# Kernel tuning notes

Hardware: AMD Instinct MI355X
Metric: run time of the kernel (lower is better)

Reference implementation:

```python
import jax, jax.numpy as jnp
import numpy as np

LN_EPS = 1e-5
RMS_EPS = 1e-5

B, T, D = 4, 2048, 1024
H, DK, DV = 4, 256, 512            # head_k_dim = D/H, head_v_dim = expand_v * head_k_dim (expand_v=2)
KDIM, VDIM = H * DK, H * DV        # 1024, 2048
FFN = 4096                          # int(d_model * ffn_ratio)
CONV = 4


def _layernorm(x, w, b):
    mu = jnp.mean(x, -1, keepdims=True)
    var = jnp.mean(jnp.square(x - mu), -1, keepdims=True)
    return (x - mu) * jax.lax.rsqrt(var + LN_EPS) * w + b


def _short_conv_silu(x, w):
    # causal depthwise conv, kernel size K, then SiLU. x: [B,T,C], w: [C,K]
    K = w.shape[1]
    xp = jnp.pad(x, ((0, 0), (K - 1, 0), (0, 0)))
    y = sum(xp[:, i:i + x.shape[1], :] * w[:, i] for i in range(K))
    return jax.nn.silu(y)


def _l2norm(x):
    return x * jax.lax.rsqrt(jnp.sum(jnp.square(x), -1, keepdims=True) + 1e-6)


def _gated_delta_rule(q, k, v, g, beta):
    # q,k: [B,T,H,DK]; v: [B,T,H,DV]; g,beta: [B,T,H]
    # S_t = exp(g_t)*S_{t-1} + k_t (beta_t*(v_t - k_t^T exp(g_t) S_{t-1}))^T ; o_t = q_t^T S_t
    def step(S, inp):
        qt, kt, vt, gt, bt = inp
        S = S * jnp.exp(gt)[..., None, None]          # [B,H,DK,DV]
        mem = jnp.einsum('bhk,bhkv->bhv', kt, S)
        delta = (vt - mem) * bt[..., None]
        S = S + jnp.einsum('bhk,bhv->bhkv', kt, delta)
        o = jnp.einsum('bhk,bhkv->bhv', qt, S)
        return S, o
    S0 = jnp.zeros((q.shape[0], H, DK, DV), q.dtype)
    xs = (q.transpose(1, 0, 2, 3), k.transpose(1, 0, 2, 3), v.transpose(1, 0, 2, 3),
          g.transpose(1, 0, 2), beta.transpose(1, 0, 2))
    _, o = jax.lax.scan(step, S0, xs)
    return o.transpose(1, 0, 2, 3)  # [B,T,H,DV]


def setup_inputs() -> dict:
    key = jax.random.key(0)
    ks = jax.random.split(key, 24)
    n = lambda k, shp, s=0.02: jax.random.normal(k, shp, dtype=jnp.float32) * s
    return {
        'x': jax.random.normal(ks[0], (B, T, D), dtype=jnp.float32),
        'Wq': n(ks[1], (D, KDIM)), 'Wk': n(ks[2], (D, KDIM)), 'Wv': n(ks[3], (D, VDIM)),
        'Wa': n(ks[4], (D, H)), 'Wb': n(ks[5], (D, H)), 'Wg': n(ks[6], (D, VDIM)),
        'conv_q_w': n(ks[7], (KDIM, CONV), 0.2), 'conv_k_w': n(ks[8], (KDIM, CONV), 0.2),
        'conv_v_w': n(ks[9], (VDIM, CONV), 0.2),
        'A_log': jnp.log(jax.random.uniform(ks[10], (H,), minval=1.0, maxval=16.0, dtype=jnp.float32)),
        'dt_bias': jax.random.uniform(ks[11], (H,), minval=0.0, maxval=0.5, dtype=jnp.float32),
        'o_norm_w': jnp.ones((DV,), jnp.float32),
        'Wo': n(ks[12], (VDIM, D)),
        'ln1_w': jnp.ones((D,), jnp.float32), 'ln1_b': jnp.zeros((D,), jnp.float32),
        'ln2_w': jnp.ones((D,), jnp.float32), 'ln2_b': jnp.zeros((D,), jnp.float32),
        'ffn_w1': n(ks[13], (D, FFN)), 'ffn_b1': jnp.zeros((FFN,), jnp.float32),
        'ffn_w2': n(ks[14], (FFN, D)), 'ffn_b2': jnp.zeros((D,), jnp.float32),
    }


def reference(x, Wq, Wk, Wv, Wa, Wb, Wg, conv_q_w, conv_k_w, conv_v_w, A_log, dt_bias,
              o_norm_w, Wo, ln1_w, ln1_b, ln2_w, ln2_b, ffn_w1, ffn_b1, ffn_w2, ffn_b2):
    normed = _layernorm(x, ln1_w, ln1_b)
    q = _short_conv_silu(normed @ Wq, conv_q_w).reshape(B, T, H, DK)
    k = _short_conv_silu(normed @ Wk, conv_k_w).reshape(B, T, H, DK)
    v = _short_conv_silu(normed @ Wv, conv_v_w).reshape(B, T, H, DV)
    q = _l2norm(q) * (DK ** -0.5)
    k = _l2norm(k)
    g = -jnp.exp(A_log) * jax.nn.softplus(normed @ Wa + dt_bias)   # [B,T,H], negative
    beta = jax.nn.sigmoid(normed @ Wb)                              # [B,T,H]
    o = _gated_delta_rule(q, k, v, g, beta)                         # [B,T,H,DV]
    gate = (normed @ Wg).reshape(B, T, H, DV)
    o = o * jax.lax.rsqrt(jnp.mean(jnp.square(o), -1, keepdims=True) + RMS_EPS)
    o = o * o_norm_w * jax.nn.silu(gate)                            # gated RMSNorm
    x = x + o.reshape(B, T, VDIM) @ Wo
    h = _layernorm(x, ln2_w, ln2_b)
    ffn = jax.nn.gelu(h @ ffn_w1 + ffn_b1, approximate=False) @ ffn_w2 + ffn_b2
    return x + ffn
```

## Files before the change

### kernel.cpp

```cpp
#include <hip/hip_runtime.h>
#include <math.h>

#define B_    4
#define T_    2048
#define D_    1024
#define H_    4
#define DK_   256
#define DV_   512
#define KDIM_ 1024
#define VDIM_ 2048
#define FFN_  4096
#define BT_   8192

typedef unsigned short bf16;
typedef __attribute__((ext_vector_type(8))) short short8;
typedef __attribute__((ext_vector_type(4))) short short4v;
typedef __attribute__((ext_vector_type(4))) float f32x4;


__device__ __forceinline__ float sigmoidf_(float x) { return 1.f / (1.f + expf(-x)); }
__device__ __forceinline__ float siluf_(float x)    { return x / (1.f + expf(-x)); }
__device__ __forceinline__ float geluf_(float x)    { return 0.5f * x * (1.f + erff(x * 0.70710678118654752f)); }

__device__ __forceinline__ float bf2f(bf16 u) {
  union { unsigned int i; float f; } c; c.i = (unsigned int)u << 16; return c.f;
}
__device__ __forceinline__ bf16 f2bf(float f) {
  union { unsigned int i; float f; } c; c.f = f;
  unsigned int r = c.i + 0x7fffu + ((c.i >> 16) & 1u);
  return (bf16)(r >> 16);
}

__device__ __forceinline__ void gload16(const bf16* g, bf16* l) {
  __builtin_amdgcn_global_load_lds((__attribute__((address_space(1))) const void*)g,
                                   (__attribute__((address_space(3))) void*)l, 16, 0, 0);
}

__device__ __forceinline__ void storeC(float* p, float v) { *p = v; }
__device__ __forceinline__ void storeC(bf16* p, float v)  { *p = f2bf(v); }

__device__ __forceinline__ short8 ld76(const bf16* p) {
  union { short8 v; short4v h[2]; } u;
  u.h[0] = *(const short4v*)p;
  u.h[1] = *(const short4v*)(p + 4);
  return u.v;
}
__device__ __forceinline__ void st4bf(bf16* p, f32x4 v) {
  short4v o;
  o[0] = (short)f2bf(v[0]); o[1] = (short)f2bf(v[1]);
  o[2] = (short)f2bf(v[2]); o[3] = (short)f2bf(v[3]);
  *(short4v*)p = o;
}

__device__ __forceinline__ float block_sum256(float v, float* red) {
#pragma unroll
  for (int off = 32; off; off >>= 1) v += __shfl_xor(v, off, 64);
  __syncthreads();
  if ((threadIdx.x & 63) == 0) red[threadIdx.x >> 6] = v;
  __syncthreads();
  return red[0] + red[1] + red[2] + red[3];
}


__global__ __launch_bounds__(256) void sentinel_kernel(float* out, int n) {
  int i = blockIdx.x * 256 + threadIdx.x;
  if (i < n) out[i] = 12345.0f;
}


__global__ __launch_bounds__(256) void ln_kernel(const float* __restrict__ x,
                                                 const float* __restrict__ w,
                                                 const float* __restrict__ b,
                                                 bf16* __restrict__ y) {
  __shared__ float red[4];
  int row = blockIdx.x;
  const float* xr = x + (size_t)row * D_;
  float xv[4];
  float s = 0.f;
#pragma unroll
  for (int i = 0; i < 4; i++) { xv[i] = xr[threadIdx.x + 256 * i]; s += xv[i]; }
  float mean = block_sum256(s, red) * (1.f / D_);
  float s2 = 0.f;
#pragma unroll
  for (int i = 0; i < 4; i++) { float d = xv[i] - mean; s2 += d * d; }
  float var = block_sum256(s2, red) * (1.f / D_);
  float inv = rsqrtf(var + 1e-5f);
  bf16* yr = y + (size_t)row * D_;
#pragma unroll
  for (int i = 0; i < 4; i++) {
    int c = threadIdx.x + 256 * i;
    yr[c] = f2bf((xv[i] - mean) * inv * w[c] + b[c]);
  }
}


__global__ __launch_bounds__(256) void convT_kernel(const float* __restrict__ src,
                                                    bf16* __restrict__ dst,
                                                    int K, int N) {
  __shared__ float t[32][33];
  int n0 = blockIdx.x * 32, k0 = blockIdx.y * 32;
  int tx = threadIdx.x & 31, ty = threadIdx.x >> 5;
#pragma unroll
  for (int i = 0; i < 4; i++)
    t[ty + i * 8][tx] = src[(size_t)(k0 + ty + i * 8) * N + n0 + tx];
  __syncthreads();
#pragma unroll
  for (int i = 0; i < 4; i++)
    dst[(size_t)(n0 + ty + i * 8) * K + k0 + tx] = f2bf(t[tx][ty + i * 8]);
}


__global__ __launch_bounds__(256) void kT_kernel(const bf16* __restrict__ k16,
                                                 bf16* __restrict__ kT) {
  __shared__ bf16 tile[32][34];
  int t0 = blockIdx.x * 32;
  int d0 = blockIdx.y * 32;
  int bh = blockIdx.z;
  int b = bh >> 2, h = bh & 3;
  int tx = threadIdx.x & 31, ty = threadIdx.x >> 5;
#pragma unroll
  for (int i = 0; i < 4; i++)
    tile[ty + 8 * i][tx] = k16[(size_t)(b * T_ + t0 + ty + 8 * i) * KDIM_ + h * DK_ + d0 + tx];
  __syncthreads();
#pragma unroll
  for (int i = 0; i < 4; i++)
    kT[((size_t)bh * DK_ + d0 + ty + 8 * i) * T_ + t0 + tx] = tile[tx][ty + 8 * i];
}


template <typename TC>
__global__ __launch_bounds__(256) void gemm_mfma(const bf16* __restrict__ A,
                                                 const bf16* __restrict__ Bt,
                                                 const float* __restrict__ bias,
                                                 const float* __restrict__ res,
                                                 TC* __restrict__ C,
                                                 int N, int K, int flags) {
  __shared__ __align__(16) bf16 As[128 * 32];
  __shared__ __align__(16) bf16 Bs[128 * 32];
  int tid = threadIdx.x;
  int wave = tid >> 6, lane = tid & 63;
  int bm = blockIdx.y * 128, bn = blockIdx.x * 128;
  int wm = (wave >> 1) * 64, wn = (wave & 1) * 64;
  int lm = lane & 15;
  int quad = lane >> 4;

  f32x4 acc[4][4];
#pragma unroll
  for (int i = 0; i < 4; i++)
#pragma unroll
    for (int j = 0; j < 4; j++) acc[i][j] = (f32x4){0.f, 0.f, 0.f, 0.f};

  int srow = wave * 32 + (lane >> 2);
  int scol = (lane & 3) * 8;
  const bf16* ag = A  + (size_t)(bm + srow) * K + scol;
  const bf16* bg = Bt + (size_t)(bn + srow) * K + scol;
  bf16* al = As + wave * 32 * 32;
  bf16* bl = Bs + wave * 32 * 32;
  const size_t gstep = (size_t)16 * K;

  for (int k0 = 0; k0 < K; k0 += 32) {
    gload16(ag + k0,         al);
    gload16(ag + k0 + gstep, al + 16 * 32);
    gload16(bg + k0,         bl);
    gload16(bg + k0 + gstep, bl + 16 * 32);
    __syncthreads();

    short8 af[4], bf[4];
#pragma unroll
    for (int i = 0; i < 4; i++)
      af[i] = *(const short8*)&As[(wm + i * 16 + lm) * 32 + quad * 8];
#pragma unroll
    for (int j = 0; j < 4; j++)
      bf[j] = *(const short8*)&Bs[(wn + j * 16 + lm) * 32 + quad * 8];
#pragma unroll
    for (int i = 0; i < 4; i++)
#pragma unroll
      for (int j = 0; j < 4; j++)
        acc[i][j] = __builtin_amdgcn_mfma_f32_16x16x32_bf16(af[i], bf[j], acc[i][j], 0, 0, 0);
    __syncthreads();
  }

#pragma unroll
  for (int i = 0; i < 4; i++) {
    int row0 = bm + wm + i * 16 + quad * 4;
#pragma unroll
    for (int j = 0; j < 4; j++) {
      int col = bn + wn + j * 16 + lm;
      float badd = (flags & 1) ? bias[col] : 0.f;
#pragma unroll
      for (int r = 0; r < 4; r++) {
        float v = acc[i][j][r] + badd;
        if (flags & 2) v = geluf_(v);
        if (flags & 4) v += res[(size_t)(row0 + r) * N + col];
        storeC(&C[(size_t)(row0 + r) * N + col], v);
      }
    }
  }
}


__global__ __launch_bounds__(256) void ab_kernel(const bf16* __restrict__ normed,
                                                 const float* __restrict__ Wa,
                                                 const float* __restrict__ Wb,
                                                 const float* __restrict__ A_log,
                                                 const float* __restrict__ dt_bias,
                                                 float* __restrict__ g,
                                                 float* __restrict__ beta) {
  __shared__ float red[4];
  int row = blockIdx.x;
  const bf16* xr = normed + (size_t)row * D_;
  float aacc[4] = {}, bacc[4] = {};
#pragma unroll
  for (int i = 0; i < 4; i++) {
    int d = threadIdx.x + 256 * i;
    float xv = bf2f(xr[d]);
    float4 wa = *(const float4*)&Wa[d * 4];
    float4 wb = *(const float4*)&Wb[d * 4];
    aacc[0] += xv * wa.x; aacc[1] += xv * wa.y; aacc[2] += xv * wa.z; aacc[3] += xv * wa.w;
    bacc[0] += xv * wb.x; bacc[1] += xv * wb.y; bacc[2] += xv * wb.z; bacc[3] += xv * wb.w;
  }
  float sa[4], sb[4];
#pragma unroll
  for (int h = 0; h < 4; h++) {
    sa[h] = block_sum256(aacc[h], red);
    sb[h] = block_sum256(bacc[h], red);
  }
  if (threadIdx.x < 4) {
    int h = threadIdx.x;
    float xa = sa[h] + dt_bias[h];
    float sp = (xa > 20.f) ? xa : log1pf(expf(xa));
    g[row * 4 + h] = -expf(A_log[h]) * sp;
    beta[row * 4 + h] = sigmoidf_(sb[h]);
  }
}


__global__ __launch_bounds__(256) void conv_qk_kernel(const float* __restrict__ pre,
                                                      const float* __restrict__ convw,
                                                      bf16* __restrict__ out,
                                                      float scale) {
  __shared__ float red[4];
  int blk = blockIdx.x;
  int h = blk & 3;
  int bt = blk >> 2;
  int t = bt & (T_ - 1);
  int c = h * DK_ + threadIdx.x;
  float y = 0.f;
#pragma unroll
  for (int i = 0; i < 4; i++) {
    int tt = t + i - 3;
    if (tt >= 0) y += pre[(size_t)(bt + i - 3) * KDIM_ + c] * convw[c * 4 + i];
  }
  y = siluf_(y);
  float ss = block_sum256(y * y, red);
  y *= rsqrtf(ss + 1e-6f) * scale;
  out[(size_t)bt * KDIM_ + c] = f2bf(y);
}

__global__ __launch_bounds__(256) void conv_v_kernel(const float* __restrict__ pre,
                                                     const float* __restrict__ convw,
                                                     bf16* __restrict__ out) {
  int idx = blockIdx.x * 256 + threadIdx.x;
  int c = idx & (VDIM_ - 1);
  int bt = idx >> 11;
  int t = bt & (T_ - 1);
  float y = 0.f;
#pragma unroll
  for (int i = 0; i < 4; i++) {
    int tt = t + i - 3;
    if (tt >= 0) y += pre[(size_t)(bt + i - 3) * VDIM_ + c] * convw[c * 4 + i];
  }
  out[idx] = f2bf(siluf_(y));
}


#define SP 76

__global__ __launch_bounds__(256, 2) void delta_p1(const bf16* __restrict__ q,
                                                   const bf16* __restrict__ k,
                                                   const bf16* __restrict__ v,
                                                   const float* __restrict__ g,
                                                   const float* __restrict__ beta,
                                                   bf16* __restrict__ Pg,
                                                   bf16* __restrict__ Wg,
                                                   bf16* __restrict__ Yg,
                                                   float* __restrict__ gsc) {
  __shared__ bf16 Abf[64 * SP];
  __shared__ bf16 DTg[64 * SP];
  __shared__ float Ub[64 * 64];
  __shared__ float Gc[64], Lm[64], Bt[64];

  int blk = blockIdx.x;
  int c = blk & 31, bh = blk >> 5;
  int b = bh >> 2, h = bh & 3;
  int tid = threadIdx.x;
  int wave = tid >> 6, lane = tid & 63;
  int lm = lane & 15, quad = lane >> 4;
  int r0 = c * 64;

  const bf16* kb = k + (size_t)b * T_ * KDIM_ + h * DK_;
  const bf16* qb = q + (size_t)b * T_ * KDIM_ + h * DK_;
  const bf16* vb = v + (size_t)b * T_ * VDIM_ + h * DV_;
  const float* gbp = g    + (size_t)b * T_ * H_ + h;
  const float* bbp = beta + (size_t)b * T_ * H_ + h;
  size_t cb = (size_t)bh * 32 + c;
  bf16* PgC = Pg + cb * 4096;
  bf16* WgC = Wg + cb * 64 * 512;
  bf16* YgC = Yg + cb * 64 * 256;

  if (wave == 0) {
    float gv = gbp[(size_t)(r0 + lane) * H_];
    float bv = bbp[(size_t)(r0 + lane) * H_];
#pragma unroll
    for (int d = 1; d < 64; d <<= 1) {
      float nn = __shfl_up(gv, (unsigned)d, 64);
      if (lane >= d) gv += nn;
    }
    Gc[lane] = gv; Lm[lane] = expf(gv); Bt[lane] = bv;
    gsc[cb * 64 + lane] = gv;
  }
  __syncthreads();

  {
    f32x4 akk[4], aqk[4];
#pragma unroll
    for (int j = 0; j < 4; j++) { akk[j] = (f32x4){0.f,0.f,0.f,0.f}; aqk[j] = (f32x4){0.f,0.f,0.f,0.f}; }
    const bf16* krow = kb + (size_t)(r0 + 16 * wave + lm) * KDIM_;
    const bf16* qrow = qb + (size_t)(r0 + 16 * wave + lm) * KDIM_;
#pragma unroll
    for (int ks = 0; ks < 8; ks++) {
      short8 ak = *(const short8*)(krow + 8 * quad + 32 * ks);
      short8 aq = *(const short8*)(qrow + 8 * quad + 32 * ks);
#pragma unroll
      for (int j = 0; j < 4; j++) {
        short8 bk = *(const short8*)(kb + (size_t)(r0 + 16 * j + lm) * KDIM_ + 8 * quad + 32 * ks);
        akk[j] = __builtin_amdgcn_mfma_f32_16x16x32_bf16(ak, bk, akk[j], 0, 0, 0);
        aqk[j] = __builtin_amdgcn_mfma_f32_16x16x32_bf16(aq, bk, aqk[j], 0, 0, 0);
      }
    }
    float gi[4], bi[4];
#pragma unroll
    for (int r = 0; r < 4; r++) {
      int i = 16 * wave + 4 * quad + r;
      gi[r] = Gc[i]; bi[r] = Bt[i];
    }
#pragma unroll
    for (int j = 0; j < 4; j++) {
      int s = 16 * j + lm;
      float gs = Gc[s];
#pragma unroll
      for (int r = 0; r < 4; r++) {
        int i = 16 * wave + 4 * quad + r;
        float dec = expf(gi[r] - gs);
        Abf[(size_t)i * SP + s] = f2bf((s < i)  ? bi[r] * dec * akk[j][r] : 0.f);
        PgC[(size_t)i * 64 + s] = f2bf((s <= i) ? dec * aqk[j][r]        : 0.f);
      }
    }
  }

  for (int grp = 0; grp < 12; grp++) {
    __syncthreads();
    {
      int* dz = (int*)DTg;
#pragma unroll
      for (int i = 0; i < 10; i++) {
        int idx = tid + 256 * i;
        if (idx < 64 * SP / 2) dz[idx] = 0;
      }
    }
    int cg = 16 * wave + lm;
#pragma unroll
    for (int ti = 0; ti < 4; ti++)
#pragma unroll
      for (int r = 0; r < 4; r++) {
        int t = 16 * ti + 4 * quad + r;
        float val;
        if (grp < 8) val = Bt[t] * bf2f(vb[(size_t)(r0 + t) * VDIM_ + grp * 64 + cg]);
        else         val = Bt[t] * Lm[t] * bf2f(kb[(size_t)(r0 + t) * KDIM_ + (grp - 8) * 64 + cg]);
        Ub[t * 64 + cg] = val;
      }
    __syncthreads();

#pragma unroll
    for (int j = 0; j < 4; j++) {
      if (j > 0) {
        f32x4 racc = (f32x4){0.f, 0.f, 0.f, 0.f};
        int nk = (j == 3) ? 2 : 1;
        for (int ks = 0; ks < nk; ks++) {
          short8 aa = ld76(&Abf[(size_t)(16 * j + lm) * SP + 8 * quad + 32 * ks]);
          short8 bd = ld76(&DTg[(size_t)(16 * wave + lm) * SP + 8 * quad + 32 * ks]);
          racc = __builtin_amdgcn_mfma_f32_16x16x32_bf16(aa, bd, racc, 0, 0, 0);
        }
#pragma unroll
        for (int r = 0; r < 4; r++)
          Ub[(16 * j + 4 * quad + r) * 64 + 16 * wave + lm] -= racc[r];
        __syncthreads();
      }
      if (wave == 0) {
        int tl = lane & 15, sg = lane >> 4;
        short4v ab4 = *(const short4v*)&Abf[(size_t)(16 * j + tl) * SP + 16 * j + 4 * sg];
        float av[4];
        av[0] = bf2f((bf16)ab4[0]); av[1] = bf2f((bf16)ab4[1]);
        av[2] = bf2f((bf16)ab4[2]); av[3] = bf2f((bf16)ab4[3]);
        float d[16];
#pragma unroll
        for (int t = 0; t < 16; t++) {
          float val = Ub[(16 * j + t) * 64 + lane];
#pragma unroll
          for (int s = 0; s < t; s++) {
            float ats = __shfl(av[s & 3], t + 16 * (s >> 2), 64);
            val -= ats * d[s];
          }
          d[t] = val;
          DTg[(size_t)lane * SP + 16 * j + t] = f2bf(val);
        }
      }
      __syncthreads();
    }

#pragma unroll
    for (int ti = 0; ti < 4; ti++)
#pragma unroll
      for (int r = 0; r < 4; r++) {
        int t = 16 * ti + 4 * quad + r;
        bf16 val = DTg[(size_t)(16 * wave + lm) * SP + t];
        if (grp < 8) WgC[(size_t)t * 512 + grp * 64 + cg] = val;
        else         YgC[(size_t)t * 256 + (grp - 8) * 64 + cg] = val;
      }
  }
}


#define SP2 264
#define SD  72

__global__ __launch_bounds__(256, 1) void delta_p2(const bf16* __restrict__ q,
                                                   const bf16* __restrict__ kT,
                                                   const bf16* __restrict__ Wg,
                                                   const bf16* __restrict__ Yg,
                                                   const bf16* __restrict__ Pg,
                                                   const float* __restrict__ gsc,
                                                   bf16* __restrict__ o) {
  __shared__ __align__(16) bf16 ST[32 * SP2];
  __shared__ __align__(16) bf16 dT[32 * SD];
  __shared__ __align__(16) bf16 dTe[32 * SD];
  __shared__ float Gc[64];
  __shared__ __align__(16) bf16 Ks[8 * 256 * 8];
  __shared__ __align__(16) bf16 Ws[64 * 32];

  int blk = blockIdx.x;
  int vs = blk & 15, bh = blk >> 4;
  int b = bh >> 2, h = bh & 3;
  int tid = threadIdx.x;
  int wave = tid >> 6, lane = tid & 63;
  int lm = lane & 15, quad = lane >> 4;
  int rt = wave;
  int v0 = vs * 32;

  const bf16* qb  = q  + (size_t)b * T_ * KDIM_ + h * DK_;
  const bf16* kTb = kT + (size_t)bh * DK_ * T_;
  bf16*       ob  = o  + (size_t)b * T_ * VDIM_ + h * DV_ + v0;

  f32x4 Sacc[4][2];
#pragma unroll
  for (int dd = 0; dd < 4; dd++)
#pragma unroll
    for (int cc = 0; cc < 2; cc++) Sacc[dd][cc] = (f32x4){0.f, 0.f, 0.f, 0.f};

  float gnext = gsc[(size_t)bh * 2048 + lane];
  short8 qfr[8], yfr[8];
  {
    const bf16* qrow = qb + (size_t)(16 * rt + lm) * KDIM_;
    const bf16* yrow = Yg + (size_t)bh * 32 * 16384 + (size_t)(16 * rt + lm) * 256;
#pragma unroll
    for (int kf = 0; kf < 8; kf++) {
      qfr[kf] = *(const short8*)(qrow + 8 * quad + 32 * kf);
      yfr[kf] = *(const short8*)(yrow + 8 * quad + 32 * kf);
    }
  }

  for (int c = 0; c < 32; c++) {
    const int r0 = c * 64;
    const size_t cb = (size_t)bh * 32 + c;

#pragma unroll
    for (int i = 0; i < 8; i++)
      gload16(kTb + (size_t)tid * T_ + r0 + i * 8, Ks + i * 2048 + wave * 512);
    gload16(Wg + cb * 32768 + (size_t)(tid >> 2) * 512 + v0 + (tid & 3) * 8, Ws + tid * 8);
    __builtin_amdgcn_sched_barrier(0);

    const bf16* pc = Pg + cb * 4096 + (size_t)(16 * rt + lm) * 64 + 8 * quad;
    short8 pfr[2];
    pfr[0] = *(const short8*)(pc);
    pfr[1] = *(const short8*)(pc + 32);
    __builtin_amdgcn_sched_barrier(0);

#pragma unroll
    for (int dd = 0; dd < 4; dd++)
#pragma unroll
      for (int cc = 0; cc < 2; cc++)
        st4bf(&ST[(size_t)(16 * cc + lm) * SP2 + 16 * (4 * wave + dd) + 4 * quad], Sacc[dd][cc]);
    Gc[lane] = gnext;
    asm volatile("s_waitcnt lgkmcnt(0)" ::: "memory");
    __builtin_amdgcn_s_barrier();

    f32x4 Yacc[2], Oacc[2];
#pragma unroll
    for (int cc = 0; cc < 2; cc++) { Yacc[cc] = (f32x4){0.f,0.f,0.f,0.f}; Oacc[cc] = (f32x4){0.f,0.f,0.f,0.f}; }
#pragma unroll
    for (int cc = 0; cc < 2; cc++) {
      short8 Bs[8];
#pragma unroll
      for (int kf = 0; kf < 8; kf++)
        Bs[kf] = *(const short8*)&ST[(size_t)(16 * cc + lm) * SP2 + 8 * quad + 32 * kf];
#pragma unroll
      for (int kf = 0; kf < 8; kf++) {
        Yacc[cc] = __builtin_amdgcn_mfma_f32_16x16x32_bf16(yfr[kf], Bs[kf], Yacc[cc], 0, 0, 0);
        Oacc[cc] = __builtin_amdgcn_mfma_f32_16x16x32_bf16(qfr[kf], Bs[kf], Oacc[cc], 0, 0, 0);
      }
    }
    __builtin_amdgcn_sched_barrier(0);

    {
      int cn = (c + 1) & 31;
      size_t cbn = (size_t)bh * 32 + cn;
      gnext = gsc[cbn * 64 + lane];
      const bf16* qrow = qb + (size_t)(cn * 64 + 16 * rt + lm) * KDIM_;
      const bf16* yrow = Yg + cbn * 16384 + (size_t)(16 * rt + lm) * 256;
#pragma unroll
      for (int kf = 0; kf < 8; kf++) {
        qfr[kf] = *(const short8*)(qrow + 8 * quad + 32 * kf);
        yfr[kf] = *(const short8*)(yrow + 8 * quad + 32 * kf);
      }
    }
    __builtin_amdgcn_sched_barrier(0);

    asm volatile("" : : "v"(*(const int*)&pfr[0]), "v"(*(const int*)&pfr[1]) : "memory");
    __builtin_amdgcn_sched_barrier(0);
    float g63 = Gc[63];
    float lamv[4], erv[4];
#pragma unroll
    for (int rr = 0; rr < 4; rr++) {
      float gr = Gc[16 * rt + 4 * quad + rr];
      lamv[rr] = __expf(gr);
      erv[rr]  = __expf(g63 - gr);
    }
#pragma unroll
    for (int cc = 0; cc < 2; cc++) {
      short4v dpack, depack;
#pragma unroll
      for (int rr = 0; rr < 4; rr++) {
        int row = 16 * rt + 4 * quad + rr;
        float dv = bf2f(Ws[row * 32 + 16 * cc + lm]) - Yacc[cc][rr];
        Oacc[cc][rr] *= lamv[rr];
        dpack[rr]  = (short)f2bf(dv);
        depack[rr] = (short)f2bf(dv * erv[rr]);
      }
      *(short4v*)&dT [(size_t)(16 * cc + lm) * SD + 16 * rt + 4 * quad] = dpack;
      *(short4v*)&dTe[(size_t)(16 * cc + lm) * SD + 16 * rt + 4 * quad] = depack;
    }
    asm volatile("s_waitcnt lgkmcnt(0)" ::: "memory");
    __builtin_amdgcn_s_barrier();

    float lend = __expf(g63);
    short8 Be[2][2];
#pragma unroll
    for (int cc = 0; cc < 2; cc++)
#pragma unroll
      for (int kf = 0; kf < 2; kf++)
        Be[cc][kf] = ld76(&dTe[(size_t)(16 * cc + lm) * SD + 8 * quad + 32 * kf]);
#pragma unroll
    for (int dd = 0; dd < 4; dd++) {
      int Dt = 4 * wave + dd;
#pragma unroll
      for (int cc = 0; cc < 2; cc++) {
        f32x4 s = Sacc[dd][cc];
        s[0] *= lend; s[1] *= lend; s[2] *= lend; s[3] *= lend;
#pragma unroll
        for (int kf = 0; kf < 2; kf++) {
          short8 ka = *(const short8*)&Ks[((size_t)(quad + 4 * kf) * 256 + 16 * Dt + lm) * 8];
          s = __builtin_amdgcn_mfma_f32_16x16x32_bf16(ka, Be[cc][kf], s, 0, 0, 0);
        }
        Sacc[dd][cc] = s;
      }
    }

#pragma unroll
    for (int cc = 0; cc < 2; cc++) {
#pragma unroll
      for (int kf = 0; kf < 2; kf++) {
        short8 bd = ld76(&dT[(size_t)(16 * cc + lm) * SD + 8 * quad + 32 * kf]);
        Oacc[cc] = __builtin_amdgcn_mfma_f32_16x16x32_bf16(pfr[kf], bd, Oacc[cc], 0, 0, 0);
      }
#pragma unroll
      for (int rr = 0; rr < 4; rr++) {
        int row = 16 * rt + 4 * quad + rr;
        ob[(size_t)(r0 + row) * VDIM_ + 16 * cc + lm] = f2bf(Oacc[cc][rr]);
      }
    }
    asm volatile("s_waitcnt lgkmcnt(0)" ::: "memory");
    __builtin_amdgcn_s_barrier();
  }
}


__global__ __launch_bounds__(256) void gated_rms_kernel(bf16* __restrict__ o,
                                                        const bf16* __restrict__ gate,
                                                        const float* __restrict__ onw) {
  __shared__ float red[4];
  int blk = blockIdx.x;
  int h = blk & 3;
  int bt = blk >> 2;
  size_t base = (size_t)bt * VDIM_ + h * DV_;
  int tid = threadIdx.x;
  float o1 = bf2f(o[base + tid]), o2 = bf2f(o[base + tid + 256]);
  float ss = block_sum256(o1 * o1 + o2 * o2, red);
  float s = rsqrtf(ss * (1.f / DV_) + 1e-5f);
  float g1 = bf2f(gate[base + tid]), g2 = bf2f(gate[base + tid + 256]);
  o[base + tid]       = f2bf(o1 * s * onw[tid] * siluf_(g1));
  o[base + tid + 256] = f2bf(o2 * s * onw[tid + 256] * siluf_(g2));
}


extern "C" void kernel_launch(void* const* d_in, const int* in_sizes, int n_in,
                              void* d_out, int out_size, void* d_ws, size_t ws_size,
                              hipStream_t stream) {
  const float* x        = (const float*)d_in[0];
  const float* Wq       = (const float*)d_in[1];
  const float* Wk       = (const float*)d_in[2];
  const float* Wv       = (const float*)d_in[3];
  const float* Wa       = (const float*)d_in[4];
  const float* Wb       = (const float*)d_in[5];
  const float* Wg       = (const float*)d_in[6];
  const float* conv_q_w = (const float*)d_in[7];
  const float* conv_k_w = (const float*)d_in[8];
  const float* conv_v_w = (const float*)d_in[9];
  const float* A_log    = (const float*)d_in[10];
  const float* dt_bias  = (const float*)d_in[11];
  const float* o_norm_w = (const float*)d_in[12];
  const float* Wo       = (const float*)d_in[13];
  const float* ln1_w    = (const float*)d_in[14];
  const float* ln1_b    = (const float*)d_in[15];
  const float* ln2_w    = (const float*)d_in[16];
  const float* ln2_b    = (const float*)d_in[17];
  const float* ffn_w1   = (const float*)d_in[18];
  const float* ffn_b1   = (const float*)d_in[19];
  const float* ffn_w2   = (const float*)d_in[20];
  const float* ffn_b2   = (const float*)d_in[21];

  size_t required = (size_t)218 << 20;
  if (ws_size < required) {
    sentinel_kernel<<<(out_size + 255) / 256, 256, 0, stream>>>((float*)d_out, out_size);
    return;
  }

  char* base = (char*)d_ws;
  float* pre    = (float*)(base);
  bf16*  normed = (bf16*)(base + ((size_t)64  << 20));
  bf16*  q16    = (bf16*)(base + ((size_t)80  << 20));
  bf16*  k16    = (bf16*)(base + ((size_t)96  << 20));
  bf16*  v16    = (bf16*)(base + ((size_t)112 << 20));
  bf16*  g16    = (bf16*)(base + ((size_t)144 << 20));
  bf16*  o16    = (bf16*)(base + ((size_t)176 << 20));
  bf16*  wslot  = (bf16*)(base + ((size_t)208 << 20));
  float* gvec   = (float*)(base + ((size_t)216 << 20));
  float* bvec   = gvec + (size_t)BT_ * H_;
  float* gsc    = (float*)(base + ((size_t)217 << 20));
  bf16*  Yg     = (bf16*)(base);
  bf16*  Wgb    = (bf16*)(base + ((size_t)16 << 20));
  bf16*  Pg     = (bf16*)(base + ((size_t)48 << 20));
  bf16*  kTg    = (bf16*)(base + ((size_t)52 << 20));
  float* x2     = (float*)(base);
  bf16*  hb16   = (bf16*)(base + ((size_t)64  << 20));
  bf16*  ffn1   = (bf16*)(base + ((size_t)80  << 20));

  ln_kernel<<<BT_, 256, 0, stream>>>(x, ln1_w, ln1_b, normed);

  convT_kernel<<<dim3(KDIM_ / 32, D_ / 32), 256, 0, stream>>>(Wq, wslot, D_, KDIM_);
  gemm_mfma<float><<<dim3(KDIM_ / 128, BT_ / 128), 256, 0, stream>>>(normed, wslot, nullptr, nullptr, pre, KDIM_, D_, 0);
  conv_qk_kernel<<<BT_ * H_, 256, 0, stream>>>(pre, conv_q_w, q16, 0.0625f);

  convT_kernel<<<dim3(KDIM_ / 32, D_ / 32), 256, 0, stream>>>(Wk, wslot, D_, KDIM_);
  gemm_mfma<float><<<dim3(KDIM_ / 128, BT_ / 128), 256, 0, stream>>>(normed, wslot, nullptr, nullptr, pre, KDIM_, D_, 0);
  conv_qk_kernel<<<BT_ * H_, 256, 0, stream>>>(pre, conv_k_w, k16, 1.0f);

  convT_kernel<<<dim3(VDIM_ / 32, D_ / 32), 256, 0, stream>>>(Wv, wslot, D_, VDIM_);
  gemm_mfma<float><<<dim3(VDIM_ / 128, BT_ / 128), 256, 0, stream>>>(normed, wslot, nullptr, nullptr, pre, VDIM_, D_, 0);
  conv_v_kernel<<<(BT_ * VDIM_) / 256, 256, 0, stream>>>(pre, conv_v_w, v16);

  convT_kernel<<<dim3(VDIM_ / 32, D_ / 32), 256, 0, stream>>>(Wg, wslot, D_, VDIM_);
  gemm_mfma<bf16><<<dim3(VDIM_ / 128, BT_ / 128), 256, 0, stream>>>(normed, wslot, nullptr, nullptr, g16, VDIM_, D_, 0);

  ab_kernel<<<BT_, 256, 0, stream>>>(normed, Wa, Wb, A_log, dt_bias, gvec, bvec);

  kT_kernel<<<dim3(T_ / 32, DK_ / 32, 16), 256, 0, stream>>>(k16, kTg);
  delta_p1<<<512, 256, 0, stream>>>(q16, k16, v16, gvec, bvec, Pg, Wgb, Yg, gsc);
  delta_p2<<<256, 256, 0, stream>>>(q16, kTg, Wgb, Yg, Pg, gsc, o16);

  gated_rms_kernel<<<BT_ * H_, 256, 0, stream>>>(o16, g16, o_norm_w);

  convT_kernel<<<dim3(D_ / 32, VDIM_ / 32), 256, 0, stream>>>(Wo, wslot, VDIM_, D_);
  gemm_mfma<float><<<dim3(D_ / 128, BT_ / 128), 256, 0, stream>>>(o16, wslot, nullptr, x, x2, D_, VDIM_, 4);

  ln_kernel<<<BT_, 256, 0, stream>>>(x2, ln2_w, ln2_b, hb16);

  convT_kernel<<<dim3(FFN_ / 32, D_ / 32), 256, 0, stream>>>(ffn_w1, wslot, D_, FFN_);
  gemm_mfma<bf16><<<dim3(FFN_ / 128, BT_ / 128), 256, 0, stream>>>(hb16, wslot, ffn_b1, nullptr, ffn1, FFN_, D_, 1 | 2);
  convT_kernel<<<dim3(D_ / 32, FFN_ / 32), 256, 0, stream>>>(ffn_w2, wslot, FFN_, D_);
  gemm_mfma<float><<<dim3(D_ / 128, BT_ / 128), 256, 0, stream>>>(ffn1, wslot, ffn_b2, x2, (float*)d_out, D_, FFN_, 1 | 4);
}
```

Before: 1.187 ms.

## Split delta_p2 value slices to 16 columns, doubling blocks and occupancy

Each delta_p2 block now owns a 16-wide slice of the value dimension instead of 32, so the grid grows from 256 to 512 blocks. Launch bounds allow two blocks per CU. Block order is changed so consecutive blocks cover different (b,h) pairs. The aim is to fill more of the MI355X CUs and overlap the serial chunk recurrence across blocks, at the price of reloading K, q, Y and P for twice as many slices and running smaller MFMA work per barrier.

```diff
diff --git a/kernel.cpp b/kernel.cpp
--- a/kernel.cpp
+++ b/kernel.cpp
@@ -434,38 +434,36 @@
 #define SP2 264
 #define SD  72
 
-__global__ __launch_bounds__(256, 1) void delta_p2(const bf16* __restrict__ q,
+__global__ __launch_bounds__(256, 2) void delta_p2(const bf16* __restrict__ q,
                                                    const bf16* __restrict__ kT,
                                                    const bf16* __restrict__ Wg,
                                                    const bf16* __restrict__ Yg,
                                                    const bf16* __restrict__ Pg,
                                                    const float* __restrict__ gsc,
                                                    bf16* __restrict__ o) {
-  __shared__ __align__(16) bf16 ST[32 * SP2];
-  __shared__ __align__(16) bf16 dT[32 * SD];
-  __shared__ __align__(16) bf16 dTe[32 * SD];
+  __shared__ __align__(16) bf16 ST[16 * SP2];
+  __shared__ __align__(16) bf16 dT[16 * SD];
+  __shared__ __align__(16) bf16 dTe[16 * SD];
   __shared__ float Gc[64];
   __shared__ __align__(16) bf16 Ks[8 * 256 * 8];
-  __shared__ __align__(16) bf16 Ws[64 * 32];
+  __shared__ __align__(16) bf16 Ws[64 * 16];
 
   int blk = blockIdx.x;
-  int vs = blk & 15, bh = blk >> 4;
+  int bh = blk & 15, vs = blk >> 4;
   int b = bh >> 2, h = bh & 3;
   int tid = threadIdx.x;
   int wave = tid >> 6, lane = tid & 63;
   int lm = lane & 15, quad = lane >> 4;
   int rt = wave;
-  int v0 = vs * 32;
+  int v0 = vs * 16;
 
   const bf16* qb  = q  + (size_t)b * T_ * KDIM_ + h * DK_;
   const bf16* kTb = kT + (size_t)bh * DK_ * T_;
   bf16*       ob  = o  + (size_t)b * T_ * VDIM_ + h * DV_ + v0;
 
-  f32x4 Sacc[4][2];
-#pragma unroll
-  for (int dd = 0; dd < 4; dd++)
-#pragma unroll
-    for (int cc = 0; cc < 2; cc++) Sacc[dd][cc] = (f32x4){0.f, 0.f, 0.f, 0.f};
+  f32x4 Sacc[4];
+#pragma unroll
+  for (int dd = 0; dd < 4; dd++) Sacc[dd] = (f32x4){0.f, 0.f, 0.f, 0.f};
 
   float gnext = gsc[(size_t)bh * 2048 + lane];
   short8 qfr[8], yfr[8];
@@ -486,7 +484,8 @@
 #pragma unroll
     for (int i = 0; i < 8; i++)
       gload16(kTb + (size_t)tid * T_ + r0 + i * 8, Ks + i * 2048 + wave * 512);
-    gload16(Wg + cb * 32768 + (size_t)(tid >> 2) * 512 + v0 + (tid & 3) * 8, Ws + tid * 8);
+    if (tid < 128)
+      gload16(Wg + cb * 32768 + (size_t)(tid >> 1) * 512 + v0 + (tid & 1) * 8, Ws + tid * 8);
     __builtin_amdgcn_sched_barrier(0);
 
     const bf16* pc = Pg + cb * 4096 + (size_t)(16 * rt + lm) * 64 + 8 * quad;
@@ -497,27 +496,21 @@
 
 #pragma unroll
     for (int dd = 0; dd < 4; dd++)
-#pragma unroll
-      for (int cc = 0; cc < 2; cc++)
-        st4bf(&ST[(size_t)(16 * cc + lm) * SP2 + 16 * (4 * wave + dd) + 4 * quad], Sacc[dd][cc]);
+      st4bf(&ST[(size_t)lm * SP2 + 16 * (4 * wave + dd) + 4 * quad], Sacc[dd]);
     Gc[lane] = gnext;
     asm volatile("s_waitcnt lgkmcnt(0)" ::: "memory");
     __builtin_amdgcn_s_barrier();
 
-    f32x4 Yacc[2], Oacc[2];
-#pragma unroll
-    for (int cc = 0; cc < 2; cc++) { Yacc[cc] = (f32x4){0.f,0.f,0.f,0.f}; Oacc[cc] = (f32x4){0.f,0.f,0.f,0.f}; }
-#pragma unroll
-    for (int cc = 0; cc < 2; cc++) {
-      short8 Bs[8];
-#pragma unroll
-      for (int kf = 0; kf < 8; kf++)
-        Bs[kf] = *(const short8*)&ST[(size_t)(16 * cc + lm) * SP2 + 8 * quad + 32 * kf];
-#pragma unroll
-      for (int kf = 0; kf < 8; kf++) {
-        Yacc[cc] = __builtin_amdgcn_mfma_f32_16x16x32_bf16(yfr[kf], Bs[kf], Yacc[cc], 0, 0, 0);
-        Oacc[cc] = __builtin_amdgcn_mfma_f32_16x16x32_bf16(qfr[kf], Bs[kf], Oacc[cc], 0, 0, 0);
-      }
+    short8 Bs[8];
+#pragma unroll
+    for (int kf = 0; kf < 8; kf++)
+      Bs[kf] = *(const short8*)&ST[(size_t)lm * SP2 + 8 * quad + 32 * kf];
+    f32x4 Yacc = (f32x4){0.f, 0.f, 0.f, 0.f};
+    f32x4 Oacc = (f32x4){0.f, 0.f, 0.f, 0.f};
+#pragma unroll
+    for (int kf = 0; kf < 8; kf++) {
+      Yacc = __builtin_amdgcn_mfma_f32_16x16x32_bf16(yfr[kf], Bs[kf], Yacc, 0, 0, 0);
+      Oacc = __builtin_amdgcn_mfma_f32_16x16x32_bf16(qfr[kf], Bs[kf], Oacc, 0, 0, 0);
     }
     __builtin_amdgcn_sched_barrier(0);
 
@@ -545,58 +538,49 @@
       lamv[rr] = __expf(gr);
       erv[rr]  = __expf(g63 - gr);
     }
-#pragma unroll
-    for (int cc = 0; cc < 2; cc++) {
+    {
       short4v dpack, depack;
 #pragma unroll
       for (int rr = 0; rr < 4; rr++) {
         int row = 16 * rt + 4 * quad + rr;
-        float dv = bf2f(Ws[row * 32 + 16 * cc + lm]) - Yacc[cc][rr];
-        Oacc[cc][rr] *= lamv[rr];
+        float dv = bf2f(Ws[row * 16 + lm]) - Yacc[rr];
+        Oacc[rr] *= lamv[rr];
         dpack[rr]  = (short)f2bf(dv);
         depack[rr] = (short)f2bf(dv * erv[rr]);
       }
-      *(short4v*)&dT [(size_t)(16 * cc + lm) * SD + 16 * rt + 4 * quad] = dpack;
-      *(short4v*)&dTe[(size_t)(16 * cc + lm) * SD + 16 * rt + 4 * quad] = depack;
+      *(short4v*)&dT [(size_t)lm * SD + 16 * rt + 4 * quad] = dpack;
+      *(short4v*)&dTe[(size_t)lm * SD + 16 * rt + 4 * quad] = depack;
     }
     asm volatile("s_waitcnt lgkmcnt(0)" ::: "memory");
     __builtin_amdgcn_s_barrier();
 
     float lend = __expf(g63);
-    short8 Be[2][2];
-#pragma unroll
-    for (int cc = 0; cc < 2; cc++)
-#pragma unroll
-      for (int kf = 0; kf < 2; kf++)
-        Be[cc][kf] = ld76(&dTe[(size_t)(16 * cc + lm) * SD + 8 * quad + 32 * kf]);
+    short8 Be[2];
+#pragma unroll
+    for (int kf = 0; kf < 2; kf++)
+      Be[kf] = ld76(&dTe[(size_t)lm * SD + 8 * quad + 32 * kf]);
 #pragma unroll
     for (int dd = 0; dd < 4; dd++) {
       int Dt = 4 * wave + dd;
-#pragma unroll
-      for (int cc = 0; cc < 2; cc++) {
-        f32x4 s = Sacc[dd][cc];
-        s[0] *= lend; s[1] *= lend; s[2] *= lend; s[3] *= lend;
-#pragma unroll
-        for (int kf = 0; kf < 2; kf++) {
-          short8 ka = *(const short8*)&Ks[((size_t)(quad + 4 * kf) * 256 + 16 * Dt + lm) * 8];
-          s = __builtin_amdgcn_mfma_f32_16x16x32_bf16(ka, Be[cc][kf], s, 0, 0, 0);
-        }
-        Sacc[dd][cc] = s;
-      }
-    }
-
-#pragma unroll
-    for (int cc = 0; cc < 2; cc++) {
+      f32x4 s = Sacc[dd];
+      s[0] *= lend; s[1] *= lend; s[2] *= lend; s[3] *= lend;
 #pragma unroll
       for (int kf = 0; kf < 2; kf++) {
-        short8 bd = ld76(&dT[(size_t)(16 * cc + lm) * SD + 8 * quad + 32 * kf]);
-        Oacc[cc] = __builtin_amdgcn_mfma_f32_16x16x32_bf16(pfr[kf], bd, Oacc[cc], 0, 0, 0);
-      }
-#pragma unroll
-      for (int rr = 0; rr < 4; rr++) {
-        int row = 16 * rt + 4 * quad + rr;
-        ob[(size_t)(r0 + row) * VDIM_ + 16 * cc + lm] = f2bf(Oacc[cc][rr]);
-      }
+        short8 ka = *(const short8*)&Ks[((size_t)(quad + 4 * kf) * 256 + 16 * Dt + lm) * 8];
+        s = __builtin_amdgcn_mfma_f32_16x16x32_bf16(ka, Be[kf], s, 0, 0, 0);
+      }
+      Sacc[dd] = s;
+    }
+
+#pragma unroll
+    for (int kf = 0; kf < 2; kf++) {
+      short8 bd = ld76(&dT[(size_t)lm * SD + 8 * quad + 32 * kf]);
+      Oacc = __builtin_amdgcn_mfma_f32_16x16x32_bf16(pfr[kf], bd, Oacc, 0, 0, 0);
+    }
+#pragma unroll
+    for (int rr = 0; rr < 4; rr++) {
+      int row = 16 * rt + 4 * quad + rr;
+      ob[(size_t)(r0 + row) * VDIM_ + lm] = f2bf(Oacc[rr]);
     }
     asm volatile("s_waitcnt lgkmcnt(0)" ::: "memory");
     __builtin_amdgcn_s_barrier();
@@ -695,7 +679,7 @@
 
   kT_kernel<<<dim3(T_ / 32, DK_ / 32, 16), 256, 0, stream>>>(k16, kTg);
   delta_p1<<<512, 256, 0, stream>>>(q16, k16, v16, gvec, bvec, Pg, Wgb, Yg, gsc);
-  delta_p2<<<256, 256, 0, stream>>>(q16, kTg, Wgb, Yg, Pg, gsc, o16);
+  delta_p2<<<512, 256, 0, stream>>>(q16, kTg, Wgb, Yg, Pg, gsc, o16);
 
   gated_rms_kernel<<<BT_ * H_, 256, 0, stream>>>(o16, g16, o_norm_w);
 
```

Measured after the change: 1.266 ms. +6.6%, slower.

## Double-buffer K and W tiles in delta_p2 and prefetch next chunk

Applied to the files above, without the earlier changes.

Ks and Ws shared-memory tiles become double-buffered, so the next chunk's K^T and W loads are issued while the current chunk computes. The P fragment and g scalars are also prefetched one chunk ahead. The block index mapping is swapped so consecutive blocks cover different batch-head pairs instead of different V slices. This is meant to hide global-load latency in the sequential chunk loop, at the cost of doubled LDS for those buffers and more live registers.

```diff
diff --git a/kernel.cpp b/kernel.cpp
--- a/kernel.cpp
+++ b/kernel.cpp
@@ -445,11 +445,11 @@
   __shared__ __align__(16) bf16 dT[32 * SD];
   __shared__ __align__(16) bf16 dTe[32 * SD];
   __shared__ float Gc[64];
-  __shared__ __align__(16) bf16 Ks[8 * 256 * 8];
-  __shared__ __align__(16) bf16 Ws[64 * 32];
+  __shared__ __align__(16) bf16 Ks[2][8 * 256 * 8];
+  __shared__ __align__(16) bf16 Ws[2][64 * 32];
 
   int blk = blockIdx.x;
-  int vs = blk & 15, bh = blk >> 4;
+  int bh = blk & 15, vs = blk >> 4;
   int b = bh >> 2, h = bh & 3;
   int tid = threadIdx.x;
   int wave = tid >> 6, lane = tid & 63;
@@ -459,6 +459,8 @@
 
   const bf16* qb  = q  + (size_t)b * T_ * KDIM_ + h * DK_;
   const bf16* kTb = kT + (size_t)bh * DK_ * T_;
+  const bf16* WgB = Wg + (size_t)bh * 32 * 32768 + (size_t)(tid >> 2) * 512 + v0 + (tid & 3) * 8;
+  const bf16* PgB = Pg + (size_t)bh * 32 * 4096 + (size_t)(16 * rt + lm) * 64 + 8 * quad;
   bf16*       ob  = o  + (size_t)b * T_ * VDIM_ + h * DV_ + v0;
 
   f32x4 Sacc[4][2];
@@ -467,7 +469,16 @@
 #pragma unroll
     for (int cc = 0; cc < 2; cc++) Sacc[dd][cc] = (f32x4){0.f, 0.f, 0.f, 0.f};
 
-  float gnext = gsc[(size_t)bh * 2048 + lane];
+#pragma unroll
+  for (int i = 0; i < 8; i++)
+    gload16(kTb + (size_t)tid * T_ + i * 8, Ks[0] + i * 2048 + wave * 512);
+  gload16(WgB, Ws[0] + tid * 8);
+  __builtin_amdgcn_sched_barrier(0);
+  short8 pfn[2];
+  pfn[0] = *(const short8*)(PgB);
+  pfn[1] = *(const short8*)(PgB + 32);
+  __builtin_amdgcn_sched_barrier(0);
+  float gnext = gsc[(size_t)bh * 2048 + lane], gnn = 0.f;
   short8 qfr[8], yfr[8];
   {
     const bf16* qrow = qb + (size_t)(16 * rt + lm) * KDIM_;
@@ -481,19 +492,11 @@
 
   for (int c = 0; c < 32; c++) {
     const int r0 = c * 64;
-    const size_t cb = (size_t)bh * 32 + c;
-
-#pragma unroll
-    for (int i = 0; i < 8; i++)
-      gload16(kTb + (size_t)tid * T_ + r0 + i * 8, Ks + i * 2048 + wave * 512);
-    gload16(Wg + cb * 32768 + (size_t)(tid >> 2) * 512 + v0 + (tid & 3) * 8, Ws + tid * 8);
-    __builtin_amdgcn_sched_barrier(0);
-
-    const bf16* pc = Pg + cb * 4096 + (size_t)(16 * rt + lm) * 64 + 8 * quad;
-    short8 pfr[2];
-    pfr[0] = *(const short8*)(pc);
-    pfr[1] = *(const short8*)(pc + 32);
-    __builtin_amdgcn_sched_barrier(0);
+    const int idx = c & 1;
+    const bf16* Ksb = Ks[idx];
+    const bf16* Wsb = Ws[idx];
+    bf16* Ksn = Ks[idx ^ 1];
+    bf16* Wsn = Ws[idx ^ 1];
 
 #pragma unroll
     for (int dd = 0; dd < 4; dd++)
@@ -523,9 +526,15 @@
 
     {
       int cn = (c + 1) & 31;
+      int rn = cn * 64;
       size_t cbn = (size_t)bh * 32 + cn;
-      gnext = gsc[cbn * 64 + lane];
-      const bf16* qrow = qb + (size_t)(cn * 64 + 16 * rt + lm) * KDIM_;
+#pragma unroll
+      for (int i = 0; i < 8; i++)
+        gload16(kTb + (size_t)tid * T_ + rn + i * 8, Ksn + i * 2048 + wave * 512);
+      gload16(WgB + (size_t)cn * 32768, Wsn + tid * 8);
+      __builtin_amdgcn_sched_barrier(0);
+      gnn = gsc[cbn * 64 + lane];
+      const bf16* qrow = qb + (size_t)(rn + 16 * rt + lm) * KDIM_;
       const bf16* yrow = Yg + cbn * 16384 + (size_t)(16 * rt + lm) * 256;
 #pragma unroll
       for (int kf = 0; kf < 8; kf++) {
@@ -535,7 +544,7 @@
     }
     __builtin_amdgcn_sched_barrier(0);
 
-    asm volatile("" : : "v"(*(const int*)&pfr[0]), "v"(*(const int*)&pfr[1]) : "memory");
+    asm volatile("" : : "v"(*(const int*)&pfn[0]), "v"(*(const int*)&pfn[1]) : "memory");
     __builtin_amdgcn_sched_barrier(0);
     float g63 = Gc[63];
     float lamv[4], erv[4];
@@ -551,7 +560,7 @@
 #pragma unroll
       for (int rr = 0; rr < 4; rr++) {
         int row = 16 * rt + 4 * quad + rr;
-        float dv = bf2f(Ws[row * 32 + 16 * cc + lm]) - Yacc[cc][rr];
+        float dv = bf2f(Wsb[row * 32 + 16 * cc + lm]) - Yacc[cc][rr];
         Oacc[cc][rr] *= lamv[rr];
         dpack[rr]  = (short)f2bf(dv);
         depack[rr] = (short)f2bf(dv * erv[rr]);
@@ -578,7 +587,7 @@
         s[0] *= lend; s[1] *= lend; s[2] *= lend; s[3] *= lend;
 #pragma unroll
         for (int kf = 0; kf < 2; kf++) {
-          short8 ka = *(const short8*)&Ks[((size_t)(quad + 4 * kf) * 256 + 16 * Dt + lm) * 8];
+          short8 ka = *(const short8*)&Ksb[((size_t)(quad + 4 * kf) * 256 + 16 * Dt + lm) * 8];
           s = __builtin_amdgcn_mfma_f32_16x16x32_bf16(ka, Be[cc][kf], s, 0, 0, 0);
         }
         Sacc[dd][cc] = s;
@@ -590,7 +599,7 @@
 #pragma unroll
       for (int kf = 0; kf < 2; kf++) {
         short8 bd = ld76(&dT[(size_t)(16 * cc + lm) * SD + 8 * quad + 32 * kf]);
-        Oacc[cc] = __builtin_amdgcn_mfma_f32_16x16x32_bf16(pfr[kf], bd, Oacc[cc], 0, 0, 0);
+        Oacc[cc] = __builtin_amdgcn_mfma_f32_16x16x32_bf16(pfn[kf], bd, Oacc[cc], 0, 0, 0);
       }
 #pragma unroll
       for (int rr = 0; rr < 4; rr++) {
@@ -598,6 +607,15 @@
         ob[(size_t)(r0 + row) * VDIM_ + 16 * cc + lm] = f2bf(Oacc[cc][rr]);
       }
     }
+    __builtin_amdgcn_sched_barrier(0);
+
+    {
+      int cn = (c + 1) & 31;
+      const bf16* pc = PgB + (size_t)cn * 4096;
+      pfn[0] = *(const short8*)(pc);
+      pfn[1] = *(const short8*)(pc + 32);
+    }
+    gnext = gnn;
     asm volatile("s_waitcnt lgkmcnt(0)" ::: "memory");
     __builtin_amdgcn_s_barrier();
   }
```

New measurement: 1.206 ms. Within noise of the previous version (+1.6%).
